# Kernel optimization log

Measured on AMD Instinct MI355X. Metric: run time of the kernel, lower is better.

## Reference

```python
import jax, jax.numpy as jnp
import numpy as np

B, S, D = 32, 256, 768
H = 12
HD = D // H           # 64
MLP = 4 * D           # 3072
EPS = 1e-5


def layernorm(x, g, b):
    mu = jnp.mean(x, axis=-1, keepdims=True)
    var = jnp.mean((x - mu) ** 2, axis=-1, keepdims=True)
    return (x - mu) * jax.lax.rsqrt(var + EPS) * g + b


def setup_inputs() -> dict:
    key = jax.random.key(0)
    ks = jax.random.split(key, 16)
    s_head = 1.0 / np.sqrt(HD)
    s_d = 1.0 / np.sqrt(D)
    s_mlp = 1.0 / np.sqrt(MLP)
    return {
        "x": jax.random.normal(ks[0], (B, S, D), dtype=jnp.float32),
        "g1": jnp.ones((D,), jnp.float32),
        "beta1": jnp.zeros((D,), jnp.float32),
        # per-head linear weights, torch Linear layout [out, in] stacked over heads
        "Wq": jax.random.uniform(ks[1], (H, HD, HD), jnp.float32, -s_head, s_head),
        "bq": jax.random.uniform(ks[2], (H, HD), jnp.float32, -s_head, s_head),
        "Wk": jax.random.uniform(ks[3], (H, HD, HD), jnp.float32, -s_head, s_head),
        "bk": jax.random.uniform(ks[4], (H, HD), jnp.float32, -s_head, s_head),
        "Wv": jax.random.uniform(ks[5], (H, HD, HD), jnp.float32, -s_head, s_head),
        "bv": jax.random.uniform(ks[6], (H, HD), jnp.float32, -s_head, s_head),
        "g2": jnp.ones((D,), jnp.float32),
        "beta2": jnp.zeros((D,), jnp.float32),
        "W1": jax.random.uniform(ks[7], (MLP, D), jnp.float32, -s_d, s_d),
        "bm1": jax.random.uniform(ks[8], (MLP,), jnp.float32, -s_d, s_d),
        "W2": jax.random.uniform(ks[9], (D, MLP), jnp.float32, -s_mlp, s_mlp),
        "bm2": jax.random.uniform(ks[10], (D,), jnp.float32, -s_mlp, s_mlp),
    }


def reference(x, g1, beta1, Wq, bq, Wk, bk, Wv, bv, g2, beta2, W1, bm1, W2, bm2):
    # --- MHA on norm1(x), fused over batch and heads ---
    h = layernorm(x, g1, beta1)                      # [B,S,D]
    hh = h.reshape(B, S, H, HD)                      # head split matches slicing in Mymha
    # q_e = sum_d hh_d * W[e,d]  (torch Linear: y = x @ W.T + b)
    q = jnp.einsum('bshd,hed->bshe', hh, Wq) + bq
    k = jnp.einsum('bshd,hed->bshe', hh, Wk) + bk
    v = jnp.einsum('bshd,hed->bshe', hh, Wv) + bv
    scores = jnp.einsum('bshe,bthe->bhst', q, k) / np.sqrt(HD)
    attn = jax.nn.softmax(scores, axis=-1)           # [B,H,S,S]
    ctx = jnp.einsum('bhst,bthe->bshe', attn, v).reshape(B, S, D)
    out = ctx + x
    # --- MLP on norm2(out) ---
    h2 = layernorm(out, g2, beta2)
    m = jax.nn.gelu(h2 @ W1.T + bm1, approximate=False)  # torch nn.GELU is exact erf
    out = m @ W2.T + bm2 + out
    return out
```

## Files before the change

### kernel.cpp

```cpp
#include <hip/hip_runtime.h>
#include <hip/hip_bf16.h>
#include <math.h>


static constexpr int Bn = 32, Sn = 256, Dn = 768, Hn = 12, HDn = 64, MLPn = 3072;
static constexpr int NT = Bn * Sn;

typedef unsigned short ushort_t;
typedef unsigned int u32;
typedef __attribute__((ext_vector_type(8))) short short8;
typedef __attribute__((ext_vector_type(4))) float f32x4;

__device__ __forceinline__ float bf2f(ushort_t u) { return __uint_as_float(((u32)u) << 16); }
__device__ __forceinline__ ushort_t f2bf(float f) {
  u32 u = __float_as_uint(f);
  u += 0x7fffu + ((u >> 16) & 1u);
  return (ushort_t)(u >> 16);
}

__device__ __forceinline__ void async_cp16(const ushort_t* g, ushort_t* l) {
  __builtin_amdgcn_global_load_lds(
      (const __attribute__((address_space(1))) u32*)g,
      (__attribute__((address_space(3))) u32*)l, 16, 0, 0);
}

__global__ __launch_bounds__(256) void k_prep(
    const float* __restrict__ Wq, const float* __restrict__ Wk,
    const float* __restrict__ Wv, const float* __restrict__ bq,
    const float* __restrict__ bk, const float* __restrict__ bv,
    const float* __restrict__ W1, const float* __restrict__ W2,
    const float* __restrict__ x, const float* __restrict__ g1,
    const float* __restrict__ be1,
    ushort_t* __restrict__ Wc, float* __restrict__ bc,
    ushort_t* __restrict__ W1b, ushort_t* __restrict__ W2b,
    ushort_t* __restrict__ hb)
{
  __shared__ float red[8];
  const int bx = blockIdx.x;
  const int tid = threadIdx.x;
  if (bx < 576) {
    int i = bx * 256 + tid;
    int h = i / 12288, rem = i - h * 12288;
    int mat = rem / 4096, w = rem - mat * 4096;
    const float* src = (mat == 0) ? Wq : ((mat == 1) ? Wk : Wv);
    Wc[i] = f2bf(src[h * 4096 + w]);
    if (i < Hn * 192) {
      int h2 = i / 192, r2 = i - h2 * 192;
      int m2 = r2 / 64, e2 = r2 - m2 * 64;
      const float* bs = (m2 == 0) ? bq : ((m2 == 1) ? bk : bv);
      bc[i] = bs[h2 * 64 + e2];
    }
  } else if (bx < 5184) {
    int j = bx - 576;
    const float* src = (j < 2304) ? W1 : W2;
    ushort_t* dst = (j < 2304) ? W1b : W2b;
    int i = (j % 2304) * 256 + tid;
    float4 v = ((const float4*)src)[i];
    ushort4 o;
    o.x = f2bf(v.x); o.y = f2bf(v.y); o.z = f2bf(v.z); o.w = f2bf(v.w);
    ((ushort4*)dst)[i] = o;
  } else {
    const int t = bx - 5184;
    float xv[3];
#pragma unroll
    for (int i = 0; i < 3; i++) xv[i] = x[(size_t)t * Dn + tid + i * 256];
    float s = xv[0] + xv[1] + xv[2];
#pragma unroll
    for (int off = 32; off > 0; off >>= 1) s += __shfl_down(s, off, 64);
    if ((tid & 63) == 0) red[tid >> 6] = s;
    __syncthreads();
    float mean = (red[0] + red[1] + red[2] + red[3]) * (1.0f / 768.0f);
    float d0 = xv[0] - mean, d1 = xv[1] - mean, d2 = xv[2] - mean;
    float s2 = d0 * d0 + d1 * d1 + d2 * d2;
#pragma unroll
    for (int off = 32; off > 0; off >>= 1) s2 += __shfl_down(s2, off, 64);
    if ((tid & 63) == 0) red[4 + (tid >> 6)] = s2;
    __syncthreads();
    float rstd = rsqrtf((red[4] + red[5] + red[6] + red[7]) * (1.0f / 768.0f) + 1e-5f);
#pragma unroll
    for (int i = 0; i < 3; i++) {
      int d = tid + i * 256;
      hb[(size_t)t * Dn + d] = f2bf((xv[i] - mean) * rstd * g1[d] + be1[d]);
    }
  }
}

__global__ __launch_bounds__(256) void k_qkv(
    const ushort_t* __restrict__ hb,
    const ushort_t* __restrict__ Wc,
    const float* __restrict__ bc,
    ushort_t* __restrict__ qo, ushort_t* __restrict__ ko, ushort_t* __restrict__ vt)
{
  __shared__ __align__(16) ushort_t As[128 * 72];
  __shared__ __align__(16) ushort_t Ws[192 * 72];
  const int blk = blockIdx.x;
  const int half = blk & 1;
  const int bh = blk >> 1;
  const int b_ = bh / Hn, h_ = bh - b_ * Hn;
  const int tid = threadIdx.x;
  const int t0 = b_ * Sn + half * 128;

  {
    int row = tid >> 1, seg = (tid & 1) * 32;
    const uint4* g = (const uint4*)(hb + (size_t)(t0 + row) * Dn + h_ * 64 + seg);
    uint4* s = (uint4*)(As + row * 72 + seg);
    s[0] = g[0]; s[1] = g[1]; s[2] = g[2]; s[3] = g[3];
  }
  {
    int rr = tid >> 2, seg = (tid & 3) * 16;
    const ushort_t* gw = Wc + h_ * 12288;
#pragma unroll
    for (int p = 0; p < 3; p++) {
      int R = p * 64 + rr;
      const uint4* g = (const uint4*)(gw + R * 64 + seg);
      uint4* s = (uint4*)(Ws + R * 72 + seg);
      s[0] = g[0]; s[1] = g[1];
    }
  }
  __syncthreads();

  const int wave = tid >> 6, lane = tid & 63;
  const int wm = (wave >> 1) * 64, wn = (wave & 1) * 96;
  const int lrow = lane & 15, quad = lane >> 4;

  f32x4 acc[4][6];
#pragma unroll
  for (int mi = 0; mi < 4; mi++)
#pragma unroll
    for (int ni = 0; ni < 6; ni++) acc[mi][ni] = (f32x4){0.f, 0.f, 0.f, 0.f};

#pragma unroll
  for (int kk = 0; kk < 2; kk++) {
    short8 af[4], wf[6];
#pragma unroll
    for (int mi = 0; mi < 4; mi++)
      af[mi] = *(const short8*)(As + (wm + mi * 16 + lrow) * 72 + kk * 32 + quad * 8);
#pragma unroll
    for (int ni = 0; ni < 6; ni++)
      wf[ni] = *(const short8*)(Ws + (wn + ni * 16 + lrow) * 72 + kk * 32 + quad * 8);
#pragma unroll
    for (int mi = 0; mi < 4; mi++)
#pragma unroll
      for (int ni = 0; ni < 6; ni++)
        acc[mi][ni] = __builtin_amdgcn_mfma_f32_16x16x32_bf16(af[mi], wf[ni], acc[mi][ni], 0, 0, 0);
  }

#pragma unroll
  for (int ni = 0; ni < 6; ni++) {
    int c = wn + ni * 16 + lrow;
    int mat = c >> 6, e = c & 63;
    float bb = bc[h_ * 192 + c];
    if (mat < 2) {
      ushort_t* dst = (mat == 0) ? qo : ko;
      size_t base = (((size_t)bh) * Sn + half * 128 + wm) * HDn + e;
#pragma unroll
      for (int mi = 0; mi < 4; mi++) {
#pragma unroll
        for (int r = 0; r < 4; r++) {
          int lr = mi * 16 + quad * 4 + r;
          dst[base + (size_t)lr * HDn] = f2bf(acc[mi][ni][r] + bb);
        }
      }
    } else {
      size_t rowb = ((size_t)bh * 64 + e) * Sn + half * 128 + wm + quad * 4;
#pragma unroll
      for (int mi = 0; mi < 4; mi++) {
        ushort4 pk;
        pk.x = f2bf(acc[mi][ni][0] + bb);
        pk.y = f2bf(acc[mi][ni][1] + bb);
        pk.z = f2bf(acc[mi][ni][2] + bb);
        pk.w = f2bf(acc[mi][ni][3] + bb);
        *(ushort4*)(vt + rowb + mi * 16) = pk;
      }
    }
  }
}

__global__ __launch_bounds__(256) void k_attn(
    const ushort_t* __restrict__ q,
    const ushort_t* __restrict__ kg_,
    const ushort_t* __restrict__ vt,
    const float* __restrict__ x,
    float* __restrict__ out1)
{
  __shared__ __align__(16) ushort_t Ks[64 * 72];
  __shared__ __align__(16) ushort_t Vts[64 * 264];
  __shared__ __align__(16) ushort_t Pw[4][16 * 72];
  const int blk = blockIdx.x;
  const int qtr = blk & 3, bh = blk >> 2;
  const int b_ = bh / Hn, h_ = bh - b_ * Hn;
  const int tid = threadIdx.x, wave = tid >> 6, lane = tid & 63;
  const int lr16 = lane & 15, quad = lane >> 4;
  const int s0 = qtr * 64 + wave * 16;

  {
    int r = tid >> 2, cseg = (tid & 3) * 64;
    const uint4* g = (const uint4*)(vt + ((size_t)bh * 64 + r) * Sn + cseg);
    uint4* s = (uint4*)(Vts + r * 264 + cseg);
#pragma unroll
    for (int i = 0; i < 8; i++) s[i] = g[i];
  }

  short8 qf[2];
  {
    const ushort_t* qg = q + ((size_t)bh * Sn + s0 + lr16) * HDn + quad * 8;
    qf[0] = *(const short8*)(qg);
    qf[1] = *(const short8*)(qg + 32);
  }

  f32x4 of[4];
#pragma unroll
  for (int et = 0; et < 4; et++) of[et] = (f32x4){0.f, 0.f, 0.f, 0.f};
  float mrow[4] = {-3.0e38f, -3.0e38f, -3.0e38f, -3.0e38f};
  float lsum[4] = {0.f, 0.f, 0.f, 0.f};

  const ushort_t* kgb = kg_ + (size_t)bh * Sn * HDn;

  for (int c = 0; c < 4; c++) {
    if (c) __syncthreads();
    {
      int row = tid >> 2, seg = (tid & 3) * 16;
      const uint4* g = (const uint4*)(kgb + (size_t)(c * 64 + row) * HDn + seg);
      uint4* s = (uint4*)(Ks + row * 72 + seg);
      s[0] = g[0]; s[1] = g[1];
    }
    __syncthreads();

    f32x4 sc[4];
#pragma unroll
    for (int ni = 0; ni < 4; ni++) sc[ni] = (f32x4){0.f, 0.f, 0.f, 0.f};
#pragma unroll
    for (int kk = 0; kk < 2; kk++) {
#pragma unroll
      for (int ni = 0; ni < 4; ni++) {
        short8 kf = *(const short8*)(Ks + (ni * 16 + lr16) * 72 + kk * 32 + quad * 8);
        sc[ni] = __builtin_amdgcn_mfma_f32_16x16x32_bf16(qf[kk], kf, sc[ni], 0, 0, 0);
      }
    }

    float alpha[4];
#pragma unroll
    for (int r = 0; r < 4; r++) {
      float m_ = fmaxf(fmaxf(sc[0][r], sc[1][r]), fmaxf(sc[2][r], sc[3][r]));
#pragma unroll
      for (int msk = 8; msk >= 1; msk >>= 1) m_ = fmaxf(m_, __shfl_xor(m_, msk, 64));
      float mn = fmaxf(mrow[r], m_);
      alpha[r] = __expf((mrow[r] - mn) * 0.125f);
      mrow[r] = mn;
    }
#pragma unroll
    for (int ni = 0; ni < 4; ni++) {
#pragma unroll
      for (int r = 0; r < 4; r++) {
        float p = __expf((sc[ni][r] - mrow[r]) * 0.125f);
        sc[ni][r] = p;
        Pw[wave][(quad * 4 + r) * 72 + ni * 16 + lr16] = f2bf(p);
      }
    }
#pragma unroll
    for (int r = 0; r < 4; r++) {
      float s_ = (sc[0][r] + sc[1][r]) + (sc[2][r] + sc[3][r]);
#pragma unroll
      for (int msk = 8; msk >= 1; msk >>= 1) s_ += __shfl_xor(s_, msk, 64);
      lsum[r] = lsum[r] * alpha[r] + s_;
    }
#pragma unroll
    for (int et = 0; et < 4; et++)
#pragma unroll
      for (int r = 0; r < 4; r++) of[et][r] *= alpha[r];

    short8 pf0 = *(const short8*)(&Pw[wave][lr16 * 72 + quad * 8]);
    short8 pf1 = *(const short8*)(&Pw[wave][lr16 * 72 + 32 + quad * 8]);
#pragma unroll
    for (int et = 0; et < 4; et++) {
      short8 vf0 = *(const short8*)(Vts + (et * 16 + lr16) * 264 + c * 64 + quad * 8);
      short8 vf1 = *(const short8*)(Vts + (et * 16 + lr16) * 264 + c * 64 + 32 + quad * 8);
      of[et] = __builtin_amdgcn_mfma_f32_16x16x32_bf16(pf0, vf0, of[et], 0, 0, 0);
      of[et] = __builtin_amdgcn_mfma_f32_16x16x32_bf16(pf1, vf1, of[et], 0, 0, 0);
    }
  }

  const size_t obase = ((size_t)b_ * Sn + s0) * Dn + h_ * 64;
#pragma unroll
  for (int r = 0; r < 4; r++) {
    float rl = 1.0f / lsum[r];
    int row = quad * 4 + r;
#pragma unroll
    for (int et = 0; et < 4; et++) {
      size_t idx = obase + (size_t)row * Dn + et * 16 + lr16;
      out1[idx] = of[et][r] * rl + x[idx];
    }
  }
}

__global__ __launch_bounds__(256) void k_ln2(
    const float* __restrict__ in, const float* __restrict__ g2,
    const float* __restrict__ be2, ushort_t* __restrict__ h2)
{
  const int t = blockIdx.x, tid = threadIdx.x;
  __shared__ float red[8];
  float xv[3];
#pragma unroll
  for (int i = 0; i < 3; i++) xv[i] = in[(size_t)t * Dn + tid + i * 256];
  float s = xv[0] + xv[1] + xv[2];
#pragma unroll
  for (int off = 32; off > 0; off >>= 1) s += __shfl_down(s, off, 64);
  if ((tid & 63) == 0) red[tid >> 6] = s;
  __syncthreads();
  float mean = (red[0] + red[1] + red[2] + red[3]) * (1.0f / 768.0f);
  float d0 = xv[0] - mean, d1 = xv[1] - mean, d2 = xv[2] - mean;
  float s2 = d0 * d0 + d1 * d1 + d2 * d2;
#pragma unroll
  for (int off = 32; off > 0; off >>= 1) s2 += __shfl_down(s2, off, 64);
  if ((tid & 63) == 0) red[4 + (tid >> 6)] = s2;
  __syncthreads();
  float rstd = rsqrtf((red[4] + red[5] + red[6] + red[7]) * (1.0f / 768.0f) + 1e-5f);
#pragma unroll
  for (int i = 0; i < 3; i++) {
    int d = tid + i * 256;
    h2[(size_t)t * Dn + d] = f2bf((xv[i] - mean) * rstd * g2[d] + be2[d]);
  }
}

__global__ __launch_bounds__(512) void k_gemm1(
    const ushort_t* __restrict__ A,
    const ushort_t* __restrict__ Bw,
    const float* __restrict__ bias,
    ushort_t* __restrict__ CoutB)
{
  constexpr int KDIM = Dn, N = MLPn;
  __shared__ __align__(16) ushort_t smem[24576];
  ushort_t* As0 = smem;
  ushort_t* Bs0 = smem + 8192;
  ushort_t* As1 = smem + 12288;
  ushort_t* Bs1 = smem + 20480;
  ushort_t* Cs = smem;
  const int b = blockIdx.x;
  const int xcd = b & 7, slot = b >> 3;
  const int cc = slot % 24, rloc = slot / 24;
  const int m0 = (xcd * 4 + rloc) * 256, n0 = cc * 128;
  const int tid = threadIdx.x;
  const int wave = tid >> 6, lane = tid & 63;
  const int wm = (wave >> 1) << 6, wn = (wave & 1) << 6;
  const int lrow = lane & 15, quad = lane >> 4;
  const int lrow4 = lane >> 2;
  const int lcol8s = (((lane & 3) ^ ((lane >> 3) & 3))) * 8;
  const int qsw = ((quad ^ ((lrow >> 1) & 3))) * 8;

  f32x4 acc[4][4];
#pragma unroll
  for (int mi = 0; mi < 4; mi++)
#pragma unroll
    for (int ni = 0; ni < 4; ni++) acc[mi][ni] = (f32x4){0.f, 0.f, 0.f, 0.f};

  auto stage = [&](int k0, ushort_t* Ad, ushort_t* Bd) {
    async_cp16(A + (size_t)(m0 + wave * 16 + lrow4) * KDIM + k0 + lcol8s,
               Ad + (wave * 16) * 32);
    async_cp16(A + (size_t)(m0 + 128 + wave * 16 + lrow4) * KDIM + k0 + lcol8s,
               Ad + (128 + wave * 16) * 32);
    async_cp16(Bw + (size_t)(n0 + wave * 16 + lrow4) * KDIM + k0 + lcol8s,
               Bd + (wave * 16) * 32);
  };
  auto compute = [&](const ushort_t* As_, const ushort_t* Bs_) {
    short8 af[4], bfv[4];
#pragma unroll
    for (int mi = 0; mi < 4; mi++)
      af[mi] = *(const short8*)(As_ + (wm + mi * 16 + lrow) * 32 + qsw);
#pragma unroll
    for (int ni = 0; ni < 4; ni++)
      bfv[ni] = *(const short8*)(Bs_ + (wn + ni * 16 + lrow) * 32 + qsw);
    __builtin_amdgcn_s_setprio(1);
#pragma unroll
    for (int mi = 0; mi < 4; mi++)
#pragma unroll
      for (int ni = 0; ni < 4; ni++)
        acc[mi][ni] = __builtin_amdgcn_mfma_f32_16x16x32_bf16(af[mi], bfv[ni], acc[mi][ni], 0, 0, 0);
    __builtin_amdgcn_s_setprio(0);
  };

  stage(0, As0, Bs0);
  stage(32, As1, Bs1);
  for (int s = 0; s < 22; s += 2) {
    __builtin_amdgcn_sched_barrier(0);
    asm volatile("s_waitcnt vmcnt(3)" ::: "memory");
    __builtin_amdgcn_s_barrier();
    __builtin_amdgcn_sched_barrier(0);
    compute(As0, Bs0);
    __builtin_amdgcn_s_barrier();
    __builtin_amdgcn_sched_barrier(0);
    stage((s + 2) * 32, As0, Bs0);
    __builtin_amdgcn_sched_barrier(0);
    asm volatile("s_waitcnt vmcnt(3)" ::: "memory");
    __builtin_amdgcn_s_barrier();
    __builtin_amdgcn_sched_barrier(0);
    compute(As1, Bs1);
    __builtin_amdgcn_s_barrier();
    __builtin_amdgcn_sched_barrier(0);
    stage((s + 3) * 32, As1, Bs1);
  }
  __builtin_amdgcn_sched_barrier(0);
  asm volatile("s_waitcnt vmcnt(3)" ::: "memory");
  __builtin_amdgcn_s_barrier();
  __builtin_amdgcn_sched_barrier(0);
  compute(As0, Bs0);
  __builtin_amdgcn_sched_barrier(0);
  asm volatile("s_waitcnt vmcnt(0)" ::: "memory");
  __builtin_amdgcn_s_barrier();
  __builtin_amdgcn_sched_barrier(0);
  compute(As1, Bs1);
  __syncthreads();

#pragma unroll
  for (int p = 0; p < 2; p++) {
    if ((wm >> 7) == p) {
#pragma unroll
      for (int ni = 0; ni < 4; ni++) {
        int col = wn + ni * 16 + lrow;
        float bc = bias[n0 + col];
#pragma unroll
        for (int mi = 0; mi < 4; mi++) {
#pragma unroll
          for (int r = 0; r < 4; r++) {
            float vv = acc[mi][ni][r] + bc;
            float u = vv * (0.7978845608f + 0.0356774081f * vv * vv);
            float o = vv / (1.0f + __expf(-2.0f * u));
            Cs[((wm & 127) + mi * 16 + quad * 4 + r) * 136 + col] = f2bf(o);
          }
        }
      }
    }
    __syncthreads();
    int row = tid >> 2, part = tid & 3;
    const uint4* s = (const uint4*)(Cs + row * 136 + part * 32);
    uint4* d = (uint4*)(CoutB + (size_t)(m0 + p * 128 + row) * N + n0 + part * 32);
#pragma unroll
    for (int i = 0; i < 4; i++) d[i] = s[i];
    if (p == 0) __syncthreads();
  }
}

__global__ __launch_bounds__(256) void k_gemm2(
    const ushort_t* __restrict__ A,
    const ushort_t* __restrict__ Bw,
    const float* __restrict__ bias,
    const float* __restrict__ res,
    float* __restrict__ out)
{
  constexpr int KDIM = MLPn, N = Dn;
  __shared__ __align__(16) ushort_t smem[24576];
  ushort_t* As0 = smem;
  ushort_t* Bs0 = smem + 4096;
  ushort_t* As1 = smem + 12288;
  ushort_t* Bs1 = smem + 16384;
  const int b = blockIdx.x;
  const int xcd = b & 7, slot = b >> 3;
  const int cc = slot % 6, rloc = slot / 6;
  const int m0 = (xcd * 16 + rloc) * 64, n0 = cc * 128;
  const int tid = threadIdx.x;
  const int wave = tid >> 6, lane = tid & 63;
  const int wm = (wave >> 1) << 5, wn = (wave & 1) << 6;
  const int lrow = lane & 15, quad = lane >> 4;
  const int r8 = lane >> 3;
  const int c8s = (((lane & 7) ^ ((lane >> 3) & 7))) * 8;
  const int qsw2[2] = { ((0 * 4 + quad) ^ (lrow & 7)) * 8,
                        ((1 * 4 + quad) ^ (lrow & 7)) * 8 };

  f32x4 acc[2][4];
#pragma unroll
  for (int mi = 0; mi < 2; mi++)
#pragma unroll
    for (int ni = 0; ni < 4; ni++) acc[mi][ni] = (f32x4){0.f, 0.f, 0.f, 0.f};

  auto stage = [&](int k0, ushort_t* Ad, ushort_t* Bd) {
    async_cp16(A + (size_t)(m0 + wave * 8 + r8) * KDIM + k0 + c8s,
               Ad + (wave * 8) * 64);
    async_cp16(A + (size_t)(m0 + 32 + wave * 8 + r8) * KDIM + k0 + c8s,
               Ad + (32 + wave * 8) * 64);
#pragma unroll
    for (int g = 0; g < 4; g++)
      async_cp16(Bw + (size_t)(n0 + g * 32 + wave * 8 + r8) * KDIM + k0 + c8s,
                 Bd + (g * 32 + wave * 8) * 64);
  };
  auto compute = [&](const ushort_t* As_, const ushort_t* Bs_) {
#pragma unroll
    for (int kk = 0; kk < 2; kk++) {
      short8 af[2], bfv[4];
#pragma unroll
      for (int mi = 0; mi < 2; mi++)
        af[mi] = *(const short8*)(As_ + (wm + mi * 16 + lrow) * 64 + qsw2[kk]);
#pragma unroll
      for (int ni = 0; ni < 4; ni++)
        bfv[ni] = *(const short8*)(Bs_ + (wn + ni * 16 + lrow) * 64 + qsw2[kk]);
      __builtin_amdgcn_s_setprio(1);
#pragma unroll
      for (int mi = 0; mi < 2; mi++)
#pragma unroll
        for (int ni = 0; ni < 4; ni++)
          acc[mi][ni] = __builtin_amdgcn_mfma_f32_16x16x32_bf16(af[mi], bfv[ni], acc[mi][ni], 0, 0, 0);
      __builtin_amdgcn_s_setprio(0);
    }
  };

  stage(0, As0, Bs0);
  stage(64, As1, Bs1);
  for (int s = 0; s < 46; s += 2) {
    __builtin_amdgcn_sched_barrier(0);
    asm volatile("s_waitcnt vmcnt(6)" ::: "memory");
    __builtin_amdgcn_s_barrier();
    __builtin_amdgcn_sched_barrier(0);
    compute(As0, Bs0);
    __builtin_amdgcn_s_barrier();
    __builtin_amdgcn_sched_barrier(0);
    stage((s + 2) * 64, As0, Bs0);
    __builtin_amdgcn_sched_barrier(0);
    asm volatile("s_waitcnt vmcnt(6)" ::: "memory");
    __builtin_amdgcn_s_barrier();
    __builtin_amdgcn_sched_barrier(0);
    compute(As1, Bs1);
    __builtin_amdgcn_s_barrier();
    __builtin_amdgcn_sched_barrier(0);
    stage((s + 3) * 64, As1, Bs1);
  }
  __builtin_amdgcn_sched_barrier(0);
  asm volatile("s_waitcnt vmcnt(6)" ::: "memory");
  __builtin_amdgcn_s_barrier();
  __builtin_amdgcn_sched_barrier(0);
  compute(As0, Bs0);
  __builtin_amdgcn_sched_barrier(0);
  asm volatile("s_waitcnt vmcnt(0)" ::: "memory");
  __builtin_amdgcn_s_barrier();
  __builtin_amdgcn_sched_barrier(0);
  compute(As1, Bs1);

#pragma unroll
  for (int ni = 0; ni < 4; ni++) {
    int col = n0 + wn + ni * 16 + lrow;
    float bc = bias[col];
#pragma unroll
    for (int mi = 0; mi < 2; mi++) {
#pragma unroll
      for (int r = 0; r < 4; r++) {
        int row = m0 + wm + mi * 16 + quad * 4 + r;
        size_t idx = (size_t)row * N + col;
        out[idx] = acc[mi][ni][r] + bc + res[idx];
      }
    }
  }
}

extern "C" void kernel_launch(void* const* d_in, const int* in_sizes, int n_in,
                              void* d_out, int out_size, void* d_ws, size_t ws_size,
                              hipStream_t stream) {
  (void)in_sizes; (void)n_in; (void)out_size; (void)ws_size;
  const float* x   = (const float*)d_in[0];
  const float* g1  = (const float*)d_in[1];
  const float* be1 = (const float*)d_in[2];
  const float* Wq  = (const float*)d_in[3];
  const float* bq  = (const float*)d_in[4];
  const float* Wk  = (const float*)d_in[5];
  const float* bk  = (const float*)d_in[6];
  const float* Wv  = (const float*)d_in[7];
  const float* bv  = (const float*)d_in[8];
  const float* g2  = (const float*)d_in[9];
  const float* be2 = (const float*)d_in[10];
  const float* W1  = (const float*)d_in[11];
  const float* bm1 = (const float*)d_in[12];
  const float* W2  = (const float*)d_in[13];
  const float* bm2 = (const float*)d_in[14];
  float* outp = (float*)d_out;

  char* ws = (char*)d_ws;
  float*    out1 = (float*)ws;
  ushort_t* hb   = (ushort_t*)ws;
  ushort_t* qb   = (ushort_t*)(ws + 25165824);
  ushort_t* kb   = (ushort_t*)(ws + 37748736);
  ushort_t* vtb  = (ushort_t*)(ws + 50331648);
  ushort_t* h2   = qb;
  ushort_t* mb   = (ushort_t*)(ws + 37748736);
  ushort_t* Wc   = (ushort_t*)(ws + 88080384);
  ushort_t* W1b  = (ushort_t*)(ws + 88375296);
  ushort_t* W2b  = (ushort_t*)(ws + 93093888);
  float*    bcb  = (float*)(ws + 97812480);

  k_prep<<<dim3(5184 + NT), dim3(256), 0, stream>>>(Wq, Wk, Wv, bq, bk, bv, W1, W2,
                                                    x, g1, be1, Wc, bcb, W1b, W2b, hb);
  k_qkv<<<dim3(Bn * Hn * 2), dim3(256), 0, stream>>>(hb, Wc, bcb, qb, kb, vtb);
  k_attn<<<dim3(Bn * Hn * 4), dim3(256), 0, stream>>>(qb, kb, vtb, x, out1);
  k_ln2<<<dim3(NT), dim3(256), 0, stream>>>(out1, g2, be2, h2);
  k_gemm1<<<dim3(768), dim3(512), 0, stream>>>(h2, W1b, bm1, mb);
  k_gemm2<<<dim3(768), dim3(256), 0, stream>>>(mb, W2b, bm2, out1, outp);
}
```

Baseline: 292.9 us.

## Enlarge GEMM1 tiles to 256x256 with quarter-staged K=64 ping-pong pipeline

```diff
diff --git a/kernel.cpp b/kernel.cpp
--- a/kernel.cpp
+++ b/kernel.cpp
@@ -322,120 +322,171 @@
   }
 }
 
-__global__ __launch_bounds__(512) void k_gemm1(
+__global__ __launch_bounds__(512, 2) void k_gemm1(
     const ushort_t* __restrict__ A,
     const ushort_t* __restrict__ Bw,
     const float* __restrict__ bias,
     ushort_t* __restrict__ CoutB)
 {
-  constexpr int KDIM = Dn, N = MLPn;
-  __shared__ __align__(16) ushort_t smem[24576];
-  ushort_t* As0 = smem;
-  ushort_t* Bs0 = smem + 8192;
-  ushort_t* As1 = smem + 12288;
-  ushort_t* Bs1 = smem + 20480;
-  ushort_t* Cs = smem;
+  constexpr int KD = Dn;
+  constexpr int NTILES = 12;
+  __shared__ __align__(16) ushort_t smem[65536];
   const int b = blockIdx.x;
   const int xcd = b & 7, slot = b >> 3;
-  const int cc = slot % 24, rloc = slot / 24;
-  const int m0 = (xcd * 4 + rloc) * 256, n0 = cc * 128;
+  const int cc = slot % 12, rloc = slot / 12;
+  const int m0 = (xcd * 4 + rloc) * 256, n0 = cc * 256;
   const int tid = threadIdx.x;
   const int wave = tid >> 6, lane = tid & 63;
-  const int wm = (wave >> 1) << 6, wn = (wave & 1) << 6;
+  const int wm2 = (wave >> 2) * 128, wn2 = (wave & 3) * 64;
   const int lrow = lane & 15, quad = lane >> 4;
-  const int lrow4 = lane >> 2;
-  const int lcol8s = (((lane & 3) ^ ((lane >> 3) & 3))) * 8;
-  const int qsw = ((quad ^ ((lrow >> 1) & 3))) * 8;
-
-  f32x4 acc[4][4];
-#pragma unroll
-  for (int mi = 0; mi < 4; mi++)
+  const int key = lrow & 7;
+
+  f32x4 acc[8][4];
+#pragma unroll
+  for (int mi = 0; mi < 8; mi++)
 #pragma unroll
     for (int ni = 0; ni < 4; ni++) acc[mi][ni] = (f32x4){0.f, 0.f, 0.f, 0.f};
 
-  auto stage = [&](int k0, ushort_t* Ad, ushort_t* Bd) {
-    async_cp16(A + (size_t)(m0 + wave * 16 + lrow4) * KDIM + k0 + lcol8s,
-               Ad + (wave * 16) * 32);
-    async_cp16(A + (size_t)(m0 + 128 + wave * 16 + lrow4) * KDIM + k0 + lcol8s,
-               Ad + (128 + wave * 16) * 32);
-    async_cp16(Bw + (size_t)(n0 + wave * 16 + lrow4) * KDIM + k0 + lcol8s,
-               Bd + (wave * 16) * 32);
+  auto stageH = [&](int ht, int part) {
+    if (ht >= NTILES) return;
+    const int k0 = ht * 64;
+    ushort_t* tb = smem + (ht & 1) * 32768 + ((part >= 2) ? 16384 : 0) + (part & 1) * 8192;
+    const ushort_t* gs = (part >= 2) ? Bw : A;
+    const int gbase = ((part >= 2) ? n0 : m0) + (part & 1) * 128;
+#pragma unroll
+    for (int j = 0; j < 2; ++j) {
+      int q = j * 512 + tid;
+      int row = q >> 3;
+      int sc = (q & 7) ^ (row & 7);
+      async_cp16(gs + (size_t)(gbase + row) * KD + k0 + sc * 8, tb + q * 8);
+    }
   };
-  auto compute = [&](const ushort_t* As_, const ushort_t* Bs_) {
-    short8 af[4], bfv[4];
-#pragma unroll
-    for (int mi = 0; mi < 4; mi++)
-      af[mi] = *(const short8*)(As_ + (wm + mi * 16 + lrow) * 32 + qsw);
-#pragma unroll
-    for (int ni = 0; ni < 4; ni++)
-      bfv[ni] = *(const short8*)(Bs_ + (wn + ni * 16 + lrow) * 32 + qsw);
-    __builtin_amdgcn_s_setprio(1);
-#pragma unroll
-    for (int mi = 0; mi < 4; mi++)
-#pragma unroll
-      for (int ni = 0; ni < 4; ni++)
-        acc[mi][ni] = __builtin_amdgcn_mfma_f32_16x16x32_bf16(af[mi], bfv[ni], acc[mi][ni], 0, 0, 0);
-    __builtin_amdgcn_s_setprio(0);
-  };
-
-  stage(0, As0, Bs0);
-  stage(32, As1, Bs1);
-  for (int s = 0; s < 22; s += 2) {
-    __builtin_amdgcn_sched_barrier(0);
-    asm volatile("s_waitcnt vmcnt(3)" ::: "memory");
-    __builtin_amdgcn_s_barrier();
-    __builtin_amdgcn_sched_barrier(0);
-    compute(As0, Bs0);
-    __builtin_amdgcn_s_barrier();
-    __builtin_amdgcn_sched_barrier(0);
-    stage((s + 2) * 32, As0, Bs0);
-    __builtin_amdgcn_sched_barrier(0);
-    asm volatile("s_waitcnt vmcnt(3)" ::: "memory");
-    __builtin_amdgcn_s_barrier();
-    __builtin_amdgcn_sched_barrier(0);
-    compute(As1, Bs1);
-    __builtin_amdgcn_s_barrier();
-    __builtin_amdgcn_sched_barrier(0);
-    stage((s + 3) * 32, As1, Bs1);
-  }
-  __builtin_amdgcn_sched_barrier(0);
-  asm volatile("s_waitcnt vmcnt(3)" ::: "memory");
+
+  stageH(0, 2); stageH(0, 0); stageH(0, 1); stageH(0, 3); stageH(1, 2); stageH(1, 0);
+  asm volatile("s_waitcnt vmcnt(4)" ::: "memory");
   __builtin_amdgcn_s_barrier();
   __builtin_amdgcn_sched_barrier(0);
-  compute(As0, Bs0);
-  __builtin_amdgcn_sched_barrier(0);
-  asm volatile("s_waitcnt vmcnt(0)" ::: "memory");
-  __builtin_amdgcn_s_barrier();
-  __builtin_amdgcn_sched_barrier(0);
-  compute(As1, Bs1);
+
+  short8 af[4][2], bl[2][2], bh[2][2];
+  for (int t = 0; t < NTILES; ++t) {
+    const ushort_t* Ab = smem + (t & 1) * 32768;
+    const ushort_t* Bb = Ab + 16384;
+
+#pragma unroll
+    for (int mi = 0; mi < 4; ++mi)
+#pragma unroll
+      for (int kk = 0; kk < 2; ++kk)
+        af[mi][kk] = *(const short8*)(Ab + (wm2 + mi * 16 + lrow) * 64 + (((kk << 2) + quad) ^ key) * 8);
+#pragma unroll
+    for (int ni = 0; ni < 2; ++ni)
+#pragma unroll
+      for (int kk = 0; kk < 2; ++kk)
+        bl[ni][kk] = *(const short8*)(Bb + (wn2 + ni * 16 + lrow) * 64 + (((kk << 2) + quad) ^ key) * 8);
+    stageH(t + 1, 1);
+    __builtin_amdgcn_s_barrier();
+    asm volatile("s_waitcnt lgkmcnt(0)" ::: "memory");
+    __builtin_amdgcn_sched_barrier(0);
+    __builtin_amdgcn_s_setprio(1);
+#pragma unroll
+    for (int kk = 0; kk < 2; ++kk)
+#pragma unroll
+      for (int mi = 0; mi < 4; ++mi)
+#pragma unroll
+        for (int ni = 0; ni < 2; ++ni)
+          acc[mi][ni] = __builtin_amdgcn_mfma_f32_16x16x32_bf16(af[mi][kk], bl[ni][kk], acc[mi][ni], 0, 0, 0);
+    __builtin_amdgcn_s_setprio(0);
+    __builtin_amdgcn_s_barrier();
+    __builtin_amdgcn_sched_barrier(0);
+
+#pragma unroll
+    for (int ni = 0; ni < 2; ++ni)
+#pragma unroll
+      for (int kk = 0; kk < 2; ++kk)
+        bh[ni][kk] = *(const short8*)(Bb + (wn2 + 32 + ni * 16 + lrow) * 64 + (((kk << 2) + quad) ^ key) * 8);
+    stageH(t + 1, 3);
+    __builtin_amdgcn_s_barrier();
+    asm volatile("s_waitcnt lgkmcnt(0)" ::: "memory");
+    __builtin_amdgcn_sched_barrier(0);
+    __builtin_amdgcn_s_setprio(1);
+#pragma unroll
+    for (int kk = 0; kk < 2; ++kk)
+#pragma unroll
+      for (int mi = 0; mi < 4; ++mi)
+#pragma unroll
+        for (int ni = 0; ni < 2; ++ni)
+          acc[mi][2 + ni] = __builtin_amdgcn_mfma_f32_16x16x32_bf16(af[mi][kk], bh[ni][kk], acc[mi][2 + ni], 0, 0, 0);
+    __builtin_amdgcn_s_setprio(0);
+    __builtin_amdgcn_s_barrier();
+    __builtin_amdgcn_sched_barrier(0);
+
+#pragma unroll
+    for (int mi = 0; mi < 4; ++mi)
+#pragma unroll
+      for (int kk = 0; kk < 2; ++kk)
+        af[mi][kk] = *(const short8*)(Ab + (wm2 + 64 + mi * 16 + lrow) * 64 + (((kk << 2) + quad) ^ key) * 8);
+    stageH(t + 2, 2);
+    __builtin_amdgcn_s_barrier();
+    asm volatile("s_waitcnt lgkmcnt(0)" ::: "memory");
+    __builtin_amdgcn_sched_barrier(0);
+    __builtin_amdgcn_s_setprio(1);
+#pragma unroll
+    for (int kk = 0; kk < 2; ++kk)
+#pragma unroll
+      for (int mi = 0; mi < 4; ++mi)
+#pragma unroll
+        for (int ni = 0; ni < 2; ++ni)
+          acc[4 + mi][2 + ni] = __builtin_amdgcn_mfma_f32_16x16x32_bf16(af[mi][kk], bh[ni][kk], acc[4 + mi][2 + ni], 0, 0, 0);
+    __builtin_amdgcn_s_setprio(0);
+    __builtin_amdgcn_s_barrier();
+    __builtin_amdgcn_sched_barrier(0);
+
+    stageH(t + 2, 0);
+    __builtin_amdgcn_s_barrier();
+    __builtin_amdgcn_s_setprio(1);
+#pragma unroll
+    for (int kk = 0; kk < 2; ++kk)
+#pragma unroll
+      for (int mi = 0; mi < 4; ++mi)
+#pragma unroll
+        for (int ni = 0; ni < 2; ++ni)
+          acc[4 + mi][ni] = __builtin_amdgcn_mfma_f32_16x16x32_bf16(af[mi][kk], bl[ni][kk], acc[4 + mi][ni], 0, 0, 0);
+    __builtin_amdgcn_s_setprio(0);
+    if (t < NTILES - 2) {
+      asm volatile("s_waitcnt vmcnt(4)" ::: "memory");
+    } else if (t == NTILES - 2) {
+      asm volatile("s_waitcnt vmcnt(0)" ::: "memory");
+    }
+    __builtin_amdgcn_s_barrier();
+    __builtin_amdgcn_sched_barrier(0);
+  }
+
+  float bwv[4];
+#pragma unroll
+  for (int ni = 0; ni < 4; ++ni) bwv[ni] = bias[n0 + wn2 + ni * 16 + lrow];
   __syncthreads();
-
-#pragma unroll
-  for (int p = 0; p < 2; p++) {
-    if ((wm >> 7) == p) {
-#pragma unroll
-      for (int ni = 0; ni < 4; ni++) {
-        int col = wn + ni * 16 + lrow;
-        float bc = bias[n0 + col];
-#pragma unroll
-        for (int mi = 0; mi < 4; mi++) {
-#pragma unroll
-          for (int r = 0; r < 4; r++) {
-            float vv = acc[mi][ni][r] + bc;
-            float u = vv * (0.7978845608f + 0.0356774081f * vv * vv);
-            float o = vv / (1.0f + __expf(-2.0f * u));
-            Cs[((wm & 127) + mi * 16 + quad * 4 + r) * 136 + col] = f2bf(o);
-          }
-        }
+#pragma unroll
+  for (int mi = 0; mi < 8; ++mi) {
+#pragma unroll
+    for (int ni = 0; ni < 4; ++ni) {
+      int col = wn2 + ni * 16 + lrow;
+#pragma unroll
+      for (int r = 0; r < 4; ++r) {
+        int row = wm2 + mi * 16 + quad * 4 + r;
+        float vv = acc[mi][ni][r] + bwv[ni];
+        float u = vv * (0.7978845608f + 0.0356774081f * vv * vv);
+        float o = vv / (1.0f + __expf(-2.0f * u));
+        int ck = (col >> 3) ^ ((row >> 2) & 7);
+        smem[row * 256 + (ck << 3) + (col & 7)] = f2bf(o);
       }
     }
-    __syncthreads();
-    int row = tid >> 2, part = tid & 3;
-    const uint4* s = (const uint4*)(Cs + row * 136 + part * 32);
-    uint4* d = (uint4*)(CoutB + (size_t)(m0 + p * 128 + row) * N + n0 + part * 32);
-#pragma unroll
-    for (int i = 0; i < 4; i++) d[i] = s[i];
-    if (p == 0) __syncthreads();
+  }
+  __syncthreads();
+#pragma unroll
+  for (int i = 0; i < 16; ++i) {
+    int idx = i * 512 + tid;
+    int rr = idx >> 5, ck = idx & 31;
+    const uint4 v = *(const uint4*)(smem + rr * 256 + ((ck ^ ((rr >> 2) & 7)) << 3));
+    *(uint4*)(CoutB + (size_t)(m0 + rr) * MLPn + n0 + ck * 8) = v;
   }
 }
 
@@ -587,6 +638,6 @@
   k_qkv<<<dim3(Bn * Hn * 2), dim3(256), 0, stream>>>(hb, Wc, bcb, qb, kb, vtb);
   k_attn<<<dim3(Bn * Hn * 4), dim3(256), 0, stream>>>(qb, kb, vtb, x, out1);
   k_ln2<<<dim3(NT), dim3(256), 0, stream>>>(out1, g2, be2, h2);
-  k_gemm1<<<dim3(768), dim3(512), 0, stream>>>(h2, W1b, bm1, mb);
+  k_gemm1<<<dim3(384), dim3(512), 0, stream>>>(h2, W1b, bm1, mb);
   k_gemm2<<<dim3(768), dim3(256), 0, stream>>>(mb, W2b, bm2, out1, outp);
 }
```

After: 287.0 us. -2.0%, faster.
